# Kernel tuning notes

Measured on AMD Instinct MI355X. Metric: run time of the kernel, lower is better.

## Reference

```python
import jax, jax.numpy as jnp
import numpy as np

HEADS = 8
DIM_HEAD = 96
INNER = HEADS * DIM_HEAD  # 768
PEP_DIM = 768
PRO_DIM = 768
SCALE = DIM_HEAD ** -0.5
NEG = -1000000.0
EPS = 1e-5


def _layer_norm(x, g, b):
    mu = jnp.mean(x, axis=-1, keepdims=True)
    var = jnp.mean(jnp.square(x - mu), axis=-1, keepdims=True)
    return (x - mu) * jax.lax.rsqrt(var + EPS) * g + b


def setup_inputs() -> dict:
    key = jax.random.key(0)
    ks = jax.random.split(key, 12)
    b, n, m = 16, 128, 2048
    peptide = jax.random.normal(ks[0], (b, n, PEP_DIM), dtype=jnp.float32)
    protein = jax.random.normal(ks[1], (b, m, PRO_DIM), dtype=jnp.float32)
    peptide_mask = jax.random.randint(ks[2], (b, n), 0, 2, dtype=jnp.int32)
    pro_mask = jax.random.randint(ks[3], (b, m), 0, 2, dtype=jnp.int32)
    s = 0.02
    Wq = jax.random.normal(ks[4], (PEP_DIM, INNER), dtype=jnp.float32) * s
    Wk = jax.random.normal(ks[5], (PRO_DIM, INNER), dtype=jnp.float32) * s
    Wv_prot = jax.random.normal(ks[6], (PRO_DIM, INNER), dtype=jnp.float32) * s
    Wv_pep = jax.random.normal(ks[7], (PEP_DIM, INNER), dtype=jnp.float32) * s
    Wo_prot = jax.random.normal(ks[8], (INNER, PEP_DIM), dtype=jnp.float32) * s
    bo_prot = jnp.zeros((PEP_DIM,), dtype=jnp.float32)
    Wo_pep = jax.random.normal(ks[9], (INNER, PRO_DIM), dtype=jnp.float32) * s
    bo_pep = jnp.zeros((PRO_DIM,), dtype=jnp.float32)
    ln_g = jnp.ones((PEP_DIM,), dtype=jnp.float32)
    ln_b = jnp.zeros((PEP_DIM,), dtype=jnp.float32)
    return {
        'peptide': peptide, 'protein': protein,
        'peptide_mask': peptide_mask, 'pro_mask': pro_mask,
        'Wq': Wq, 'Wk': Wk, 'Wv_prot': Wv_prot, 'Wv_pep': Wv_pep,
        'Wo_prot': Wo_prot, 'bo_prot': bo_prot,
        'Wo_pep': Wo_pep, 'bo_pep': bo_pep,
        'ln_g': ln_g, 'ln_b': ln_b,
    }


def reference(peptide, protein, peptide_mask, pro_mask,
              Wq, Wk, Wv_prot, Wv_pep, Wo_prot, bo_prot, Wo_pep, bo_pep,
              ln_g, ln_b):
    b, n, _ = peptide.shape
    m = protein.shape[1]
    # projections -> (b, h, len, d)
    q = (peptide @ Wq).reshape(b, n, HEADS, DIM_HEAD).transpose(0, 2, 1, 3)
    k = (protein @ Wk).reshape(b, m, HEADS, DIM_HEAD).transpose(0, 2, 1, 3)
    v_prot = (protein @ Wv_prot).reshape(b, m, HEADS, DIM_HEAD).transpose(0, 2, 1, 3)
    v_pep = (peptide @ Wv_pep).reshape(b, n, HEADS, DIM_HEAD).transpose(0, 2, 1, 3)
    # scores (b, h, n, m)
    dots = jnp.einsum('bhnd,bhmd->bhnm', q, k) * SCALE
    dots = jnp.where(peptide_mask[:, None, :, None] == 0, NEG, dots)
    dots = jnp.where(pro_mask[:, None, None, :] == 0, NEG, dots)
    attn = jax.nn.softmax(dots, axis=-1)
    # peptide-side output: rows of attn aggregate protein values
    out_protein = jnp.einsum('bhnm,bhmd->bhnd', attn, v_prot)
    out_protein = out_protein.transpose(0, 2, 1, 3).reshape(b, n, INNER)
    out_protein = out_protein @ Wo_prot + bo_prot
    out_protein = _layer_norm(out_protein + peptide, ln_g, ln_b)
    # protein-side output: attn^T aggregates peptide values
    out_peptide = jnp.einsum('bhnm,bhnd->bhmd', attn, v_pep)
    out_peptide = out_peptide.transpose(0, 2, 1, 3).reshape(b, m, INNER)
    out_peptide = out_peptide @ Wo_pep + bo_pep
    out_peptide = _layer_norm(out_peptide + protein, ln_g, ln_b)
    return (out_protein, out_peptide, attn)
```

## Files before the change

kernel.cpp:

```cpp
#include <hip/hip_runtime.h>
#include <math.h>

static constexpr int HEADS  = 8;
static constexpr int DHEAD  = 96;
static constexpr int INNER  = 768;
static constexpr int NPEP   = 128;
static constexpr int MPRO   = 2048;
static constexpr float ATT_SCALE = 0.10206207261596577f;
static constexpr float NEGF   = -1000000.0f;
static constexpr float LN_EPS = 1e-5f;

typedef __attribute__((ext_vector_type(8))) short bf16x8;
typedef __attribute__((ext_vector_type(4))) float f32x4;

__device__ __forceinline__ unsigned short f2b(float f) {
    unsigned u = __builtin_bit_cast(unsigned, f);
    u += 0x7fffu + ((u >> 16) & 1u);
    return (unsigned short)(u >> 16);
}
__device__ __forceinline__ float b2f(unsigned short u) {
    return __builtin_bit_cast(float, (unsigned)u << 16);
}

__device__ __forceinline__ void async16(const unsigned short* g, unsigned short* l) {
    __builtin_amdgcn_global_load_lds(
        (const __attribute__((address_space(1))) void*)g,
        (__attribute__((address_space(3))) void*)l, 16, 0, 0);
}

template<int TM, int MODE>
__global__ __launch_bounds__(256) void gemm_bf16(
    const unsigned short* __restrict__ A, const unsigned short* __restrict__ B,
    unsigned short* __restrict__ C,
    int M, int N, int K, int lda, int ldb, int ldc,
    long sAb, long sAh, long sBb, long sBh, long sCb, long sCh,
    const int* __restrict__ mRow, const int* __restrict__ mCol, int lenShift,
    int nxSwz)
{
    (void)mRow; (void)mCol; (void)M;
    constexpr int FR   = TM / 32;
    constexpr int PIPE = 3;
    __shared__ unsigned short As[PIPE][TM * 32];
    __shared__ unsigned short Bs[PIPE][128 * 32];

    const int tid = threadIdx.x;
    int bx, by;
    if (nxSwz > 0) {
        const int bid = blockIdx.x;
        const int per = gridDim.x >> 3;
        const int v   = (bid & 7) * per + (bid >> 3);
        bx = v % nxSwz; by = v / nxSwz;
    } else { bx = blockIdx.x; by = blockIdx.y; }
    const int n0  = bx * 128;
    const int m0  = by * TM;
    const int z   = blockIdx.z;
    const int zb  = z >> 3, zh = z & 7;

    const unsigned short* Ab = A + zb * sAb + zh * sAh;
    const unsigned short* Bb = B + zb * sBb + zh * sBh;

    const int rS = tid >> 2;
    const int kS = (tid & 3) * 8;
    const int wave = tid >> 6;

    const int lane = tid & 63;
    const int l16  = lane & 15;
    const int quad = lane >> 4;
    const int wr   = (wave >> 1) * (TM / 2);
    const int wc   = (wave & 1) * 64;

    f32x4 acc[FR][4];
#pragma unroll
    for (int i = 0; i < FR; ++i)
#pragma unroll
        for (int j = 0; j < 4; ++j) acc[i][j] = (f32x4){0.f, 0.f, 0.f, 0.f};

    auto stageT = [&](int t, int bi) {
        const int k0 = t << 5;
        unsigned short* a0 = &As[bi][wave * 512];
        async16(Ab + (long)(m0 + rS) * lda + k0 + kS, a0);
        if (TM == 128)
            async16(Ab + (long)(m0 + 64 + rS) * lda + k0 + kS, a0 + 2048);
        int bR0 = n0 + rS;      if (bR0 > N - 1) bR0 = N - 1;
        int bR1 = n0 + 64 + rS; if (bR1 > N - 1) bR1 = N - 1;
        unsigned short* b0 = &Bs[bi][wave * 512];
        async16(Bb + (long)bR0 * ldb + k0 + kS, b0);
        async16(Bb + (long)bR1 * ldb + k0 + kS, b0 + 2048);
    };

    const int NT = K >> 5;
    stageT(0, 0);
    if (NT > 1) stageT(1, 1);
    if (NT > 2) stageT(2, 2);

    int bi = 0;
    for (int t = 0; t < NT; ++t) {
        const int ahead = NT - 1 - t;
        if constexpr (TM == 128) {
            if (ahead >= 2)      asm volatile("s_waitcnt vmcnt(8)" ::: "memory");
            else if (ahead == 1) asm volatile("s_waitcnt vmcnt(4)" ::: "memory");
            else                 asm volatile("s_waitcnt vmcnt(0)" ::: "memory");
        } else {
            if (ahead >= 2)      asm volatile("s_waitcnt vmcnt(6)" ::: "memory");
            else if (ahead == 1) asm volatile("s_waitcnt vmcnt(3)" ::: "memory");
            else                 asm volatile("s_waitcnt vmcnt(0)" ::: "memory");
        }
        __builtin_amdgcn_s_barrier();

        bf16x8 af[FR], bfr[4];
#pragma unroll
        for (int i = 0; i < FR; ++i)
            af[i] = *reinterpret_cast<const bf16x8*>(&As[bi][(wr + i * 16 + l16) * 32 + quad * 8]);
#pragma unroll
        for (int j = 0; j < 4; ++j)
            bfr[j] = *reinterpret_cast<const bf16x8*>(&Bs[bi][(wc + j * 16 + l16) * 32 + quad * 8]);

        __builtin_amdgcn_s_setprio(1);
#pragma unroll
        for (int i = 0; i < FR; ++i)
#pragma unroll
            for (int j = 0; j < 4; ++j)
                acc[i][j] = __builtin_amdgcn_mfma_f32_16x16x32_bf16(af[i], bfr[j], acc[i][j], 0, 0, 0);
        __builtin_amdgcn_s_setprio(0);

        __builtin_amdgcn_s_barrier();
        __builtin_amdgcn_sched_barrier(0);
        if (t + PIPE < NT) stageT(t + PIPE, bi);
        bi = bi + 1; if (bi == PIPE) bi = 0;
    }

#pragma unroll
    for (int i = 0; i < FR; ++i) {
#pragma unroll
        for (int j = 0; j < 4; ++j) {
            const int col = n0 + wc + j * 16 + l16;
            if ((MODE == 2) && col >= N) continue;
            const int h = col / 96, d = col - h * 96;
#pragma unroll
            for (int r = 0; r < 4; ++r) {
                const int row = m0 + wr + i * 16 + quad * 4 + r;
                float v = acc[i][j][r];
                if (MODE == 1) {
                    v *= ATT_SCALE;
                    C[zb * sCb + zh * sCh + (long)row * ldc + col] = f2b(v);
                } else if (MODE == 2) {
                    C[zb * sCb + zh * sCh + (long)row * ldc + col] = f2b(v);
                } else if (MODE == 3) {
                    const int b = row >> lenShift, rr = row & ((1 << lenShift) - 1);
                    C[(((long)(b * 8 + h) << lenShift) + rr) * 96 + d] = f2b(v);
                } else {
                    const int b = row >> lenShift, rr = row & ((1 << lenShift) - 1);
                    C[(((long)(b * 8 + h) * 96 + d) << lenShift) + rr] = f2b(v);
                }
            }
        }
    }
}

__global__ __launch_bounds__(256) void pv2_kernel(
    const unsigned short* __restrict__ attn16,
    const unsigned short* __restrict__ vpepT,
    unsigned short* __restrict__ opep)
{
    __shared__ unsigned short At[128 * 136];
    __shared__ unsigned short Bv[128 * 136];

    const int tid = threadIdx.x;
    const int m0  = blockIdx.x * 128;
    const int z   = blockIdx.y;
    const int b   = z >> 3, h = z & 7;

    const unsigned short* Az = attn16 + (long)z * NPEP * MPRO;
    const unsigned short* Bz = vpepT + (long)z * 96 * 128;

    {
        const int r = tid >> 1, half = tid & 1;
        const int rc = r > 95 ? 95 : r;
#pragma unroll
        for (int e = 0; e < 8; ++e) {
            bf16x8 v = *reinterpret_cast<const bf16x8*>(Bz + rc * 128 + half * 64 + e * 8);
            *reinterpret_cast<bf16x8*>(&Bv[r * 136 + half * 64 + e * 8]) = v;
        }
    }
    {
        const int mBase = (tid & 7) * 16;
#pragma unroll
        for (int nn = 0; nn < 128; nn += 32) {
            const int n = nn + (tid >> 3);
#pragma unroll
            for (int c = 0; c < 2; ++c) {
                bf16x8 v = *reinterpret_cast<const bf16x8*>(Az + (long)n * MPRO + m0 + mBase + c * 8);
#pragma unroll
                for (int j = 0; j < 8; ++j)
                    At[(mBase + c * 8 + j) * 136 + n] = (unsigned short)v[j];
            }
        }
    }
    __syncthreads();

    const int lane = tid & 63;
    const int l16  = lane & 15;
    const int quad = lane >> 4;
    const int wave = tid >> 6;
    const int wr   = (wave >> 1) * 64;
    const int wc   = (wave & 1) * 64;

    f32x4 acc[4][4];
#pragma unroll
    for (int i = 0; i < 4; ++i)
#pragma unroll
        for (int j = 0; j < 4; ++j) acc[i][j] = (f32x4){0.f, 0.f, 0.f, 0.f};

#pragma unroll
    for (int kc = 0; kc < 4; ++kc) {
        bf16x8 af[4], bfr[4];
#pragma unroll
        for (int i = 0; i < 4; ++i)
            af[i] = *reinterpret_cast<const bf16x8*>(&At[(wr + i * 16 + l16) * 136 + kc * 32 + quad * 8]);
#pragma unroll
        for (int j = 0; j < 4; ++j)
            bfr[j] = *reinterpret_cast<const bf16x8*>(&Bv[(wc + j * 16 + l16) * 136 + kc * 32 + quad * 8]);
#pragma unroll
        for (int i = 0; i < 4; ++i)
#pragma unroll
            for (int j = 0; j < 4; ++j)
                acc[i][j] = __builtin_amdgcn_mfma_f32_16x16x32_bf16(af[i], bfr[j], acc[i][j], 0, 0, 0);
    }

#pragma unroll
    for (int i = 0; i < 4; ++i) {
#pragma unroll
        for (int j = 0; j < 4; ++j) {
            const int d = wc + j * 16 + l16;
            if (d >= 96) continue;
#pragma unroll
            for (int r = 0; r < 4; ++r) {
                const int m = m0 + wr + i * 16 + quad * 4 + r;
                opep[(long)b * MPRO * INNER + (long)m * INNER + h * 96 + d] = f2b(acc[i][j][r]);
            }
        }
    }
}

__global__ __launch_bounds__(256) void conv2_kernel(
    const float* __restrict__ pro, const float* __restrict__ pep,
    unsigned short* __restrict__ pro16, unsigned short* __restrict__ pep16,
    int nPro4, int nPep4)
{
    const int i = blockIdx.x * 256 + threadIdx.x;
    const float* in; unsigned short* out; int idx;
    if (i < nPro4) { in = pro; out = pro16; idx = i; }
    else { idx = i - nPro4; if (idx >= nPep4) return; in = pep; out = pep16; }
    float4 v = reinterpret_cast<const float4*>(in)[idx];
    ushort4 o;
    o.x = f2b(v.x); o.y = f2b(v.y); o.z = f2b(v.z); o.w = f2b(v.w);
    reinterpret_cast<ushort4*>(out)[idx] = o;
}

__global__ __launch_bounds__(256) void wtrans_kernel(
    const float* w0, const float* w1, const float* w2,
    const float* w3, const float* w4, const float* w5,
    unsigned short* o0, unsigned short* o1, unsigned short* o2,
    unsigned short* o3, unsigned short* o4, unsigned short* o5)
{
    const float* in; unsigned short* out;
    switch (blockIdx.z) {
        case 0: in = w0; out = o0; break;
        case 1: in = w1; out = o1; break;
        case 2: in = w2; out = o2; break;
        case 3: in = w3; out = o3; break;
        case 4: in = w4; out = o4; break;
        default: in = w5; out = o5; break;
    }
    __shared__ unsigned short t[32][33];
    const int bx = blockIdx.x * 32, by = blockIdx.y * 32;
    const int x = threadIdx.x, y = threadIdx.y;
#pragma unroll
    for (int i = 0; i < 32; i += 8)
        t[y + i][x] = f2b(in[(long)(by + y + i) * 768 + bx + x]);
    __syncthreads();
#pragma unroll
    for (int i = 0; i < 32; i += 8)
        out[(long)(bx + y + i) * 768 + by + x] = t[x][y + i];
}

__global__ __launch_bounds__(256) void softmax_kernel(
    unsigned short* __restrict__ s16, float* __restrict__ attn,
    const int* __restrict__ pepm, const int* __restrict__ prom)
{
    __shared__ float smx[4], sms[4];
    const long row = blockIdx.x;
    const int b = (int)(row >> 10);
    const int n = (int)(row & 127);
    unsigned short* p16 = s16 + row * (long)MPRO;
    float* pf = attn + row * (long)MPRO;
    const int tid = threadIdx.x;
    const int wv = tid >> 6;
    const int rowOk = pepm[(b << 7) + n];

    float v[8];
    float mx = -3.4e38f;
    if (rowOk) {
#pragma unroll
        for (int k = 0; k < 8; ++k) {
            const int c = tid + k * 256;
            float x = b2f(p16[c]);
            if (prom[(b << 11) + c] == 0) x = NEGF;
            v[k] = x; mx = fmaxf(mx, x);
        }
    } else {
#pragma unroll
        for (int k = 0; k < 8; ++k) v[k] = NEGF;
        mx = NEGF;
    }
#pragma unroll
    for (int off = 32; off > 0; off >>= 1) mx = fmaxf(mx, __shfl_xor(mx, off));
    if ((tid & 63) == 0) smx[wv] = mx;
    __syncthreads();
    mx = fmaxf(fmaxf(smx[0], smx[1]), fmaxf(smx[2], smx[3]));

    float sum = 0.f;
#pragma unroll
    for (int k = 0; k < 8; ++k) { v[k] = __expf(v[k] - mx); sum += v[k]; }
#pragma unroll
    for (int off = 32; off > 0; off >>= 1) sum += __shfl_xor(sum, off);
    if ((tid & 63) == 0) sms[wv] = sum;
    __syncthreads();
    const float inv = 1.0f / (sms[0] + sms[1] + sms[2] + sms[3]);
#pragma unroll
    for (int k = 0; k < 8; ++k) {
        const float o = v[k] * inv;
        pf[tid + k * 256] = o;
        p16[tid + k * 256] = f2b(o);
    }
}

__global__ __launch_bounds__(256) void bias_res_ln(
    const unsigned short* __restrict__ tmp, const float* __restrict__ bias,
    const float* __restrict__ res, const float* __restrict__ gam,
    const float* __restrict__ bet, float* __restrict__ out)
{
    __shared__ float red[8];
    const long row = blockIdx.x;
    const unsigned short* t = tmp + row * INNER;
    const float* r = res + row * INNER;
    float* o = out + row * INNER;
    const int tid = threadIdx.x;
    const int wv = tid >> 6;

    float v[3]; float s = 0.f;
#pragma unroll
    for (int k = 0; k < 3; ++k) { const int c = tid + k * 256; v[k] = b2f(t[c]) + bias[c] + r[c]; s += v[k]; }
#pragma unroll
    for (int off = 32; off > 0; off >>= 1) s += __shfl_xor(s, off);
    if ((tid & 63) == 0) red[wv] = s;
    __syncthreads();
    const float mu = (red[0] + red[1] + red[2] + red[3]) * (1.0f / INNER);

    float vs = 0.f;
#pragma unroll
    for (int k = 0; k < 3; ++k) { const float d = v[k] - mu; vs += d * d; }
#pragma unroll
    for (int off = 32; off > 0; off >>= 1) vs += __shfl_xor(vs, off);
    if ((tid & 63) == 0) red[4 + wv] = vs;
    __syncthreads();
    const float rstd = rsqrtf((red[4] + red[5] + red[6] + red[7]) * (1.0f / INNER) + LN_EPS);
#pragma unroll
    for (int k = 0; k < 3; ++k) { const int c = tid + k * 256; o[c] = (v[k] - mu) * rstd * gam[c] + bet[c]; }
}

extern "C" void kernel_launch(void* const* d_in, const int* in_sizes, int n_in,
                              void* d_out, int out_size, void* d_ws, size_t ws_size,
                              hipStream_t stream)
{
    (void)in_sizes; (void)n_in; (void)out_size; (void)ws_size;

    const float* peptide = (const float*)d_in[0];
    const float* protein = (const float*)d_in[1];
    const int*   pepm    = (const int*)  d_in[2];
    const int*   prom    = (const int*)  d_in[3];
    const float* Wq      = (const float*)d_in[4];
    const float* Wk      = (const float*)d_in[5];
    const float* Wv_prot = (const float*)d_in[6];
    const float* Wv_pep  = (const float*)d_in[7];
    const float* Wo_prot = (const float*)d_in[8];
    const float* bo_prot = (const float*)d_in[9];
    const float* Wo_pep  = (const float*)d_in[10];
    const float* bo_pep  = (const float*)d_in[11];
    const float* ln_g    = (const float*)d_in[12];
    const float* ln_b    = (const float*)d_in[13];

    char* ws = (char*)d_ws;
    auto U = [&](size_t off) { return (unsigned short*)(ws + off); };
    unsigned short* WT0   = U(0);
    unsigned short* WT1   = U(1179648);
    unsigned short* WT2   = U(2 * 1179648);
    unsigned short* WT3   = U(3 * 1179648);
    unsigned short* WT4   = U(4 * 1179648);
    unsigned short* WT5   = U(5 * 1179648);
    unsigned short* q16   = U(7077888);
    unsigned short* k16   = U(10223616);
    unsigned short* vpT   = U(60555264);
    unsigned short* vpepT = U(110886912);
    unsigned short* s16   = U(114032640);
    unsigned short* pro16 = U(114032640);
    unsigned short* pep16 = U(164364288);
    unsigned short* opp   = U(7077888);
    unsigned short* tmp1  = U(10223616);
    unsigned short* opep  = U(13369344);
    unsigned short* tmp2  = U(63700992);

    float* outP = (float*)d_out;
    float* outQ = outP + 16 * 128 * 768;
    float* attn = outQ + (long)16 * 2048 * 768;

    conv2_kernel<<<26112, 256, 0, stream>>>(protein, peptide, pro16, pep16, 6291456, 393216);
    wtrans_kernel<<<dim3(24, 24, 6), dim3(32, 8), 0, stream>>>(
        Wq, Wk, Wv_prot, Wv_pep, Wo_prot, Wo_pep, WT0, WT1, WT2, WT3, WT4, WT5);

    gemm_bf16<128, 3><<<dim3(6, 16, 1), 256, 0, stream>>>(
        pep16, WT0, q16, 2048, 768, 768, 768, 768, 0,
        0, 0, 0, 0, 0, 0, nullptr, nullptr, 7, 0);
    gemm_bf16<128, 3><<<dim3(1536, 1, 1), 256, 0, stream>>>(
        pro16, WT1, k16, 32768, 768, 768, 768, 768, 0,
        0, 0, 0, 0, 0, 0, nullptr, nullptr, 11, 6);
    gemm_bf16<128, 4><<<dim3(1536, 1, 1), 256, 0, stream>>>(
        pro16, WT2, vpT, 32768, 768, 768, 768, 768, 0,
        0, 0, 0, 0, 0, 0, nullptr, nullptr, 11, 6);
    gemm_bf16<128, 4><<<dim3(6, 16, 1), 256, 0, stream>>>(
        pep16, WT3, vpepT, 2048, 768, 768, 768, 768, 0,
        0, 0, 0, 0, 0, 0, nullptr, nullptr, 7, 0);

    gemm_bf16<128, 1><<<dim3(16, 1, 128), 256, 0, stream>>>(
        q16, k16, s16, 128, 2048, 96, 96, 96, 2048,
        98304L, 12288L, 1572864L, 196608L, 2097152L, 262144L, nullptr, nullptr, 0, 0);

    softmax_kernel<<<16384, 256, 0, stream>>>(s16, attn, pepm, prom);

    gemm_bf16<64, 2><<<dim3(1, 2, 128), 256, 0, stream>>>(
        s16, vpT, opp, 128, 96, 2048, 2048, 2048, 768,
        2097152L, 262144L, 1572864L, 196608L, 98304L, 96L, nullptr, nullptr, 0, 0);

    gemm_bf16<64, 2><<<dim3(6, 32, 1), 256, 0, stream>>>(
        opp, WT4, tmp1, 2048, 768, 768, 768, 768, 768,
        0, 0, 0, 0, 0, 0, nullptr, nullptr, 0, 0);
    bias_res_ln<<<2048, 256, 0, stream>>>(tmp1, bo_prot, peptide, ln_g, ln_b, outP);

    pv2_kernel<<<dim3(16, 128), 256, 0, stream>>>(s16, vpepT, opep);

    gemm_bf16<128, 2><<<dim3(1536, 1, 1), 256, 0, stream>>>(
        opep, WT5, tmp2, 32768, 768, 768, 768, 768, 768,
        0, 0, 0, 0, 0, 0, nullptr, nullptr, 0, 6);
    bias_res_ln<<<32768, 256, 0, stream>>>(tmp2, bo_pep, protein, ln_g, ln_b, outQ);
}
```

Baseline: 754.1 us.

## Fuse K/V projection GEMMs and merge both attention-value products into one kernel

The K and V_prot projections (and Q and V_pep) now run as a single GEMM launch with a new mode that routes the upper column half to a second weight and output layout, so the shared input is read in one pass over a doubled grid. The separate attn·V_prot GEMM and the attn^T·V_pep kernel are replaced by one fused kernel of 256 blocks. Each block streams its head's attention rows once, accumulating the peptide-side output and computing the protein-side output for the chunks it owns. This aims to cut launches and re-reads of the large attention matrix. The cost is a low block count for the fused kernel, global fragment loads without LDS staging, and extra barriers.

Measured after the change: 752.6 us. About the same (-0.2%).

```diff
diff --git a/kernel.cpp b/kernel.cpp
--- a/kernel.cpp
+++ b/kernel.cpp
@@ -34,10 +34,10 @@
     unsigned short* __restrict__ C,
     int M, int N, int K, int lda, int ldb, int ldc,
     long sAb, long sAh, long sBb, long sBh, long sCb, long sCh,
-    const int* __restrict__ mRow, const int* __restrict__ mCol, int lenShift,
-    int nxSwz)
-{
-    (void)mRow; (void)mCol; (void)M;
+    int lenShift, int nxSwz,
+    const unsigned short* __restrict__ B2, unsigned short* __restrict__ C2)
+{
+    (void)M;
     constexpr int FR   = TM / 32;
     constexpr int PIPE = 3;
     __shared__ unsigned short As[PIPE][TM * 32];
@@ -51,13 +51,16 @@
         const int v   = (bid & 7) * per + (bid >> 3);
         bx = v % nxSwz; by = v / nxSwz;
     } else { bx = blockIdx.x; by = blockIdx.y; }
-    const int n0  = bx * 128;
+    int n0        = bx * 128;
     const int m0  = by * TM;
     const int z   = blockIdx.z;
     const int zb  = z >> 3, zh = z & 7;
 
+    bool sideB = false;
+    if (MODE == 5 && n0 >= 768) { sideB = true; n0 -= 768; }
+
     const unsigned short* Ab = A + zb * sAb + zh * sAh;
-    const unsigned short* Bb = B + zb * sBb + zh * sBh;
+    const unsigned short* Bb = ((MODE == 5 && sideB) ? B2 : B) + zb * sBb + zh * sBh;
 
     const int rS = tid >> 2;
     const int kS = (tid & 3) * 8;
@@ -146,100 +149,165 @@
                 } else if (MODE == 2) {
                     C[zb * sCb + zh * sCh + (long)row * ldc + col] = f2b(v);
                 } else if (MODE == 3) {
-                    const int b = row >> lenShift, rr = row & ((1 << lenShift) - 1);
-                    C[(((long)(b * 8 + h) << lenShift) + rr) * 96 + d] = f2b(v);
+                    const int bb = row >> lenShift, rr = row & ((1 << lenShift) - 1);
+                    C[(((long)(bb * 8 + h) << lenShift) + rr) * 96 + d] = f2b(v);
+                } else if (MODE == 4) {
+                    const int bb = row >> lenShift, rr = row & ((1 << lenShift) - 1);
+                    C[(((long)(bb * 8 + h) * 96 + d) << lenShift) + rr] = f2b(v);
                 } else {
-                    const int b = row >> lenShift, rr = row & ((1 << lenShift) - 1);
-                    C[(((long)(b * 8 + h) * 96 + d) << lenShift) + rr] = f2b(v);
+                    const int bb = row >> lenShift, rr = row & ((1 << lenShift) - 1);
+                    if (!sideB)
+                        C [(((long)(bb * 8 + h) << lenShift) + rr) * 96 + d] = f2b(v);
+                    else
+                        C2[(((long)(bb * 8 + h) * 96 + d) << lenShift) + rr] = f2b(v);
                 }
             }
         }
     }
 }
 
-__global__ __launch_bounds__(256) void pv2_kernel(
+__global__ __launch_bounds__(256) void fusedpv_kernel(
     const unsigned short* __restrict__ attn16,
+    const unsigned short* __restrict__ vprotT,
     const unsigned short* __restrict__ vpepT,
+    unsigned short* __restrict__ opp,
     unsigned short* __restrict__ opep)
 {
-    __shared__ unsigned short At[128 * 136];
-    __shared__ unsigned short Bv[128 * 136];
-
-    const int tid = threadIdx.x;
-    const int m0  = blockIdx.x * 128;
-    const int z   = blockIdx.y;
-    const int b   = z >> 3, h = z & 7;
+    __shared__ unsigned short AttT[128 * 136];
+    __shared__ unsigned short Vp[96 * 136];
+
+    const int id = blockIdx.x;
+    const int z  = ((id >> 4) << 3) + (id & 7);
+    const int nh = (id >> 3) & 1;
+    const int b  = z >> 3, h = z & 7;
 
     const unsigned short* Az = attn16 + (long)z * NPEP * MPRO;
-    const unsigned short* Bz = vpepT + (long)z * 96 * 128;
-
-    {
-        const int r = tid >> 1, half = tid & 1;
-        const int rc = r > 95 ? 95 : r;
-#pragma unroll
-        for (int e = 0; e < 8; ++e) {
-            bf16x8 v = *reinterpret_cast<const bf16x8*>(Bz + rc * 128 + half * 64 + e * 8);
-            *reinterpret_cast<bf16x8*>(&Bv[r * 136 + half * 64 + e * 8]) = v;
-        }
-    }
-    {
-        const int mBase = (tid & 7) * 16;
-#pragma unroll
-        for (int nn = 0; nn < 128; nn += 32) {
-            const int n = nn + (tid >> 3);
-#pragma unroll
-            for (int c = 0; c < 2; ++c) {
-                bf16x8 v = *reinterpret_cast<const bf16x8*>(Az + (long)n * MPRO + m0 + mBase + c * 8);
-#pragma unroll
-                for (int j = 0; j < 8; ++j)
-                    At[(mBase + c * 8 + j) * 136 + n] = (unsigned short)v[j];
-            }
-        }
-    }
-    __syncthreads();
-
+    const unsigned short* Vz = vprotT + (long)z * 96 * MPRO;
+    const unsigned short* Pz = vpepT  + (long)z * 96 * 128;
+
+    const int tid  = threadIdx.x;
     const int lane = tid & 63;
     const int l16  = lane & 15;
     const int quad = lane >> 4;
     const int wave = tid >> 6;
-    const int wr   = (wave >> 1) * 64;
-    const int wc   = (wave & 1) * 64;
-
-    f32x4 acc[4][4];
-#pragma unroll
-    for (int i = 0; i < 4; ++i)
-#pragma unroll
-        for (int j = 0; j < 4; ++j) acc[i][j] = (f32x4){0.f, 0.f, 0.f, 0.f};
-
-#pragma unroll
-    for (int kc = 0; kc < 4; ++kc) {
-        bf16x8 af[4], bfr[4];
-#pragma unroll
-        for (int i = 0; i < 4; ++i)
-            af[i] = *reinterpret_cast<const bf16x8*>(&At[(wr + i * 16 + l16) * 136 + kc * 32 + quad * 8]);
-#pragma unroll
-        for (int j = 0; j < 4; ++j)
-            bfr[j] = *reinterpret_cast<const bf16x8*>(&Bv[(wc + j * 16 + l16) * 136 + kc * 32 + quad * 8]);
-#pragma unroll
-        for (int i = 0; i < 4; ++i)
-#pragma unroll
-            for (int j = 0; j < 4; ++j)
-                acc[i][j] = __builtin_amdgcn_mfma_f32_16x16x32_bf16(af[i], bfr[j], acc[i][j], 0, 0, 0);
-    }
-
-#pragma unroll
-    for (int i = 0; i < 4; ++i) {
-#pragma unroll
-        for (int j = 0; j < 4; ++j) {
-            const int d = wc + j * 16 + l16;
-            if (d >= 96) continue;
+    const int wrN  = (wave >> 1) * 32;
+    const int wrM  = (wave >> 1) * 64;
+    const int wcD  = (wave & 1) * 48;
+
+#pragma unroll
+    for (int e = 0; e < 6; ++e) {
+        const int c = tid + e * 256;
+        const int row = c >> 4, coloff = (c & 15) * 8;
+        bf16x8 v = *reinterpret_cast<const bf16x8*>(Pz + row * 128 + coloff);
+        *reinterpret_cast<bf16x8*>(&Vp[row * 136 + coloff]) = v;
+    }
+    __syncthreads();
+
+    f32x4 acc1[2][3];
+#pragma unroll
+    for (int i = 0; i < 2; ++i)
+#pragma unroll
+        for (int j = 0; j < 3; ++j) acc1[i][j] = (f32x4){0.f, 0.f, 0.f, 0.f};
+
+    for (int cc = 0; cc < 16; ++cc) {
+        const int m0 = cc * 128;
+        const bool own = (cc >> 3) == nh;
+
+        bf16x8 a1[2][4], b1[3][4];
+#pragma unroll
+        for (int i = 0; i < 2; ++i) {
+            const int n = nh * 64 + wrN + i * 16 + l16;
+#pragma unroll
+            for (int kc = 0; kc < 4; ++kc)
+                a1[i][kc] = *reinterpret_cast<const bf16x8*>(
+                    Az + (long)n * MPRO + m0 + kc * 32 + quad * 8);
+        }
+#pragma unroll
+        for (int j = 0; j < 3; ++j) {
+            const int d = wcD + j * 16 + l16;
+#pragma unroll
+            for (int kc = 0; kc < 4; ++kc)
+                b1[j][kc] = *reinterpret_cast<const bf16x8*>(
+                    Vz + (long)d * MPRO + m0 + kc * 32 + quad * 8);
+        }
+
+        if (own) {
+            const int mBase = (tid & 7) * 16;
+#pragma unroll
+            for (int nn = 0; nn < 128; nn += 32) {
+                const int n = nn + (tid >> 3);
+#pragma unroll
+                for (int c = 0; c < 2; ++c) {
+                    bf16x8 v = *reinterpret_cast<const bf16x8*>(
+                        Az + (long)n * MPRO + m0 + mBase + c * 8);
+#pragma unroll
+                    for (int jj = 0; jj < 8; ++jj)
+                        AttT[(mBase + c * 8 + jj) * 136 + n] = (unsigned short)v[jj];
+                }
+            }
+            __syncthreads();
+        }
+
+#pragma unroll
+        for (int kc = 0; kc < 4; ++kc)
+#pragma unroll
+            for (int i = 0; i < 2; ++i)
+#pragma unroll
+                for (int j = 0; j < 3; ++j)
+                    acc1[i][j] = __builtin_amdgcn_mfma_f32_16x16x32_bf16(
+                        a1[i][kc], b1[j][kc], acc1[i][j], 0, 0, 0);
+
+        if (own) {
+            f32x4 acc2[4][3];
+#pragma unroll
+            for (int i = 0; i < 4; ++i)
+#pragma unroll
+                for (int j = 0; j < 3; ++j) acc2[i][j] = (f32x4){0.f, 0.f, 0.f, 0.f};
+#pragma unroll
+            for (int kc = 0; kc < 4; ++kc) {
+                bf16x8 a2[4], b2v[3];
+#pragma unroll
+                for (int i = 0; i < 4; ++i)
+                    a2[i] = *reinterpret_cast<const bf16x8*>(
+                        &AttT[(wrM + i * 16 + l16) * 136 + kc * 32 + quad * 8]);
+#pragma unroll
+                for (int j = 0; j < 3; ++j)
+                    b2v[j] = *reinterpret_cast<const bf16x8*>(
+                        &Vp[(wcD + j * 16 + l16) * 136 + kc * 32 + quad * 8]);
+#pragma unroll
+                for (int i = 0; i < 4; ++i)
+#pragma unroll
+                    for (int j = 0; j < 3; ++j)
+                        acc2[i][j] = __builtin_amdgcn_mfma_f32_16x16x32_bf16(
+                            a2[i], b2v[j], acc2[i][j], 0, 0, 0);
+            }
+#pragma unroll
+            for (int i = 0; i < 4; ++i)
+#pragma unroll
+                for (int j = 0; j < 3; ++j) {
+                    const int d = wcD + j * 16 + l16;
+#pragma unroll
+                    for (int r = 0; r < 4; ++r) {
+                        const int m = m0 + wrM + i * 16 + quad * 4 + r;
+                        opep[(long)b * MPRO * INNER + (long)m * INNER + h * 96 + d]
+                            = f2b(acc2[i][j][r]);
+                    }
+                }
+            __syncthreads();
+        }
+    }
+
+#pragma unroll
+    for (int i = 0; i < 2; ++i)
+#pragma unroll
+        for (int j = 0; j < 3; ++j) {
+            const int d = wcD + j * 16 + l16;
 #pragma unroll
             for (int r = 0; r < 4; ++r) {
-                const int m = m0 + wr + i * 16 + quad * 4 + r;
-                opep[(long)b * MPRO * INNER + (long)m * INNER + h * 96 + d] = f2b(acc[i][j][r]);
+                const int n = nh * 64 + wrN + i * 16 + quad * 4 + r;
+                opp[((long)b * NPEP + n) * INNER + h * 96 + d] = f2b(acc1[i][j][r]);
             }
         }
-    }
 }
 
 __global__ __launch_bounds__(256) void conv2_kernel(
@@ -406,8 +474,8 @@
     unsigned short* pro16 = U(114032640);
     unsigned short* pep16 = U(164364288);
     unsigned short* opp   = U(7077888);
-    unsigned short* tmp1  = U(10223616);
-    unsigned short* opep  = U(13369344);
+    unsigned short* opep  = U(10223616);
+    unsigned short* tmp1  = U(164364288);
     unsigned short* tmp2  = U(63700992);
 
     float* outP = (float*)d_out;
@@ -418,38 +486,28 @@
     wtrans_kernel<<<dim3(24, 24, 6), dim3(32, 8), 0, stream>>>(
         Wq, Wk, Wv_prot, Wv_pep, Wo_prot, Wo_pep, WT0, WT1, WT2, WT3, WT4, WT5);
 
-    gemm_bf16<128, 3><<<dim3(6, 16, 1), 256, 0, stream>>>(
+    gemm_bf16<128, 5><<<dim3(12, 16, 1), 256, 0, stream>>>(
         pep16, WT0, q16, 2048, 768, 768, 768, 768, 0,
-        0, 0, 0, 0, 0, 0, nullptr, nullptr, 7, 0);
-    gemm_bf16<128, 3><<<dim3(1536, 1, 1), 256, 0, stream>>>(
+        0, 0, 0, 0, 0, 0, 7, 0, WT3, vpepT);
+    gemm_bf16<128, 5><<<dim3(3072, 1, 1), 256, 0, stream>>>(
         pro16, WT1, k16, 32768, 768, 768, 768, 768, 0,
-        0, 0, 0, 0, 0, 0, nullptr, nullptr, 11, 6);
-    gemm_bf16<128, 4><<<dim3(1536, 1, 1), 256, 0, stream>>>(
-        pro16, WT2, vpT, 32768, 768, 768, 768, 768, 0,
-        0, 0, 0, 0, 0, 0, nullptr, nullptr, 11, 6);
-    gemm_bf16<128, 4><<<dim3(6, 16, 1), 256, 0, stream>>>(
-        pep16, WT3, vpepT, 2048, 768, 768, 768, 768, 0,
-        0, 0, 0, 0, 0, 0, nullptr, nullptr, 7, 0);
+        0, 0, 0, 0, 0, 0, 11, 12, WT2, vpT);
 
     gemm_bf16<128, 1><<<dim3(16, 1, 128), 256, 0, stream>>>(
         q16, k16, s16, 128, 2048, 96, 96, 96, 2048,
-        98304L, 12288L, 1572864L, 196608L, 2097152L, 262144L, nullptr, nullptr, 0, 0);
+        98304L, 12288L, 1572864L, 196608L, 2097152L, 262144L, 0, 0, nullptr, nullptr);
 
     softmax_kernel<<<16384, 256, 0, stream>>>(s16, attn, pepm, prom);
 
-    gemm_bf16<64, 2><<<dim3(1, 2, 128), 256, 0, stream>>>(
-        s16, vpT, opp, 128, 96, 2048, 2048, 2048, 768,
-        2097152L, 262144L, 1572864L, 196608L, 98304L, 96L, nullptr, nullptr, 0, 0);
+    fusedpv_kernel<<<256, 256, 0, stream>>>(s16, vpT, vpepT, opp, opep);
 
     gemm_bf16<64, 2><<<dim3(6, 32, 1), 256, 0, stream>>>(
         opp, WT4, tmp1, 2048, 768, 768, 768, 768, 768,
-        0, 0, 0, 0, 0, 0, nullptr, nullptr, 0, 0);
+        0, 0, 0, 0, 0, 0, 0, 0, nullptr, nullptr);
     bias_res_ln<<<2048, 256, 0, stream>>>(tmp1, bo_prot, peptide, ln_g, ln_b, outP);
-
-    pv2_kernel<<<dim3(16, 128), 256, 0, stream>>>(s16, vpepT, opep);
 
     gemm_bf16<128, 2><<<dim3(1536, 1, 1), 256, 0, stream>>>(
         opep, WT5, tmp2, 32768, 768, 768, 768, 768, 768,
-        0, 0, 0, 0, 0, 0, nullptr, nullptr, 0, 6);
+        0, 0, 0, 0, 0, 0, 0, 6, nullptr, nullptr);
     bias_res_ln<<<32768, 256, 0, stream>>>(tmp2, bo_pep, protein, ln_g, ln_b, outQ);
 }
```
